# Optimization experiments

Hardware: AMD Instinct MI355X
Metric: run time of the kernel (lower is better)

The kernel has to match this reference:

```python
import jax, jax.numpy as jnp
import numpy as np

STAGE_NUM = 5
BETA = 1.0
EPS = 1e-6


def _em_refine(cls, proto):
    # cls: [b, d]; proto: [k, d]. Matches torch einsum('bd,bkd->bk') with
    # batch-replicated prototypes == cls @ proto.T (no (b,k,d) materialization).
    p = proto
    for _ in range(STAGE_NUM):
        r = jax.nn.softmax(cls @ p.T, axis=1)          # [b, k]
        p = r.T @ cls                                   # [k, d]
        p = p / (jnp.linalg.norm(p, axis=1, keepdims=True) + EPS)
    return p


def setup_inputs() -> dict:
    key = jax.random.key(0)
    k1, k2 = jax.random.split(key)
    b, d, k = 8192, 1024, 512
    cls = jax.random.normal(k1, (b, d), dtype=jnp.float32)
    proto = jax.random.normal(k2, (k, d), dtype=jnp.float32)
    # __init__ normalizes prototypes to unit norm (with 1e-6 in denominator)
    proto = proto / (1e-6 + jnp.linalg.norm(proto, axis=1, keepdims=True))
    return {"cls": cls, "prototypes": proto}


def reference(cls, prototypes):
    # EM loop runs under torch.no_grad() -> stop_gradient here.
    new_proto = jax.lax.stop_gradient(_em_refine(cls, prototypes))  # [k, d]
    dot = cls @ new_proto.T                                          # [b, k]
    r = jax.nn.softmax(dot, axis=1)
    z_recon = r @ new_proto                                          # [b, d]
    z_out = BETA * z_recon + cls
    return (r, z_out)
```

## Files before the change

### kernel.cpp

```cpp
#include <hip/hip_runtime.h>

typedef short v8s __attribute__((ext_vector_type(8)));
typedef _Float16 v8h __attribute__((ext_vector_type(8)));
typedef float v4f __attribute__((ext_vector_type(4)));

typedef __attribute__((address_space(1))) const void* as1_void_cp;
typedef __attribute__((address_space(3))) void* as3_void_p;

__device__ __forceinline__ unsigned short f2bf(float x) {
  union { float f; unsigned int u; } v; v.f = x;
  unsigned int r = v.u + 0x7fffu + ((v.u >> 16) & 1u);
  return (unsigned short)(r >> 16);
}
__device__ __forceinline__ float bf2f(unsigned short h) {
  union { unsigned int u; float f; } v; v.u = ((unsigned int)h) << 16;
  return v.f;
}
__device__ __forceinline__ unsigned short f2h(float x) {
  _Float16 h = (_Float16)x;
  return __builtin_bit_cast(unsigned short, h);
}

template <bool ADD, bool F16>
__global__ __launch_bounds__(256) void gemm_bt(
    const unsigned short* __restrict__ A, const unsigned short* __restrict__ B,
    float* __restrict__ C, const float* __restrict__ Cadd,
    int N, int lda, int ldb, int klen, size_t csplit) {
  __shared__ __align__(16) unsigned short As[128 * 64];
  __shared__ __align__(16) unsigned short Bs[128 * 64];
  const int tid = threadIdx.x;
  const int bn = blockIdx.x * 128, bm = blockIdx.y * 128;
  const int k0 = blockIdx.z * klen;
  float* Cp = C + (size_t)blockIdx.z * csplit;

  const unsigned short* ag0 = A + (size_t)(bm + (tid >> 2)) * lda + ((tid & 3) << 3) + k0;
  const unsigned short* ag1 = ag0 + (size_t)64 * lda;
  const unsigned short* bg0 = B + (size_t)(bn + (tid >> 2)) * ldb + ((tid & 3) << 3) + k0;
  const unsigned short* bg1 = bg0 + (size_t)64 * ldb;
  unsigned short* al0 = As + tid * 8;
  unsigned short* al1 = As + 2048 + tid * 8;
  unsigned short* al2 = As + 4096 + tid * 8;
  unsigned short* al3 = As + 6144 + tid * 8;
  unsigned short* bl0 = Bs + tid * 8;
  unsigned short* bl1 = Bs + 2048 + tid * 8;
  unsigned short* bl2 = Bs + 4096 + tid * 8;
  unsigned short* bl3 = Bs + 6144 + tid * 8;

  const int lane = tid & 63;
  const int q = lane >> 4, m15 = lane & 15;
  const int w = tid >> 6;
  const int wr = (w >> 1) * 64, wc = (w & 1) * 64;

  v4f acc[4][4];
#pragma unroll
  for (int i = 0; i < 4; ++i)
#pragma unroll
    for (int j = 0; j < 4; ++j) acc[i][j] = 0.f;

  for (int kk = 0; kk < klen; kk += 64) {
    __builtin_amdgcn_global_load_lds((as1_void_cp)(ag0 + kk), (as3_void_p)al0, 16, 0, 0);
    __builtin_amdgcn_global_load_lds((as1_void_cp)(ag1 + kk), (as3_void_p)al1, 16, 0, 0);
    __builtin_amdgcn_global_load_lds((as1_void_cp)(ag0 + kk + 32), (as3_void_p)al2, 16, 0, 0);
    __builtin_amdgcn_global_load_lds((as1_void_cp)(ag1 + kk + 32), (as3_void_p)al3, 16, 0, 0);
    __builtin_amdgcn_global_load_lds((as1_void_cp)(bg0 + kk), (as3_void_p)bl0, 16, 0, 0);
    __builtin_amdgcn_global_load_lds((as1_void_cp)(bg1 + kk), (as3_void_p)bl1, 16, 0, 0);
    __builtin_amdgcn_global_load_lds((as1_void_cp)(bg0 + kk + 32), (as3_void_p)bl2, 16, 0, 0);
    __builtin_amdgcn_global_load_lds((as1_void_cp)(bg1 + kk + 32), (as3_void_p)bl3, 16, 0, 0);
    __syncthreads();
#pragma unroll
    for (int h = 0; h < 2; ++h) {
      v8s af[4], bf[4];
#pragma unroll
      for (int i = 0; i < 4; ++i)
        af[i] = *(const v8s*)(As + h * 4096 + (wr + i * 16 + m15) * 32 + q * 8);
#pragma unroll
      for (int j = 0; j < 4; ++j)
        bf[j] = *(const v8s*)(Bs + h * 4096 + (wc + j * 16 + m15) * 32 + q * 8);
#pragma unroll
      for (int i = 0; i < 4; ++i)
#pragma unroll
        for (int j = 0; j < 4; ++j) {
          if constexpr (F16)
            acc[i][j] = __builtin_amdgcn_mfma_f32_16x16x32_f16(
                __builtin_bit_cast(v8h, af[i]), __builtin_bit_cast(v8h, bf[j]), acc[i][j], 0, 0, 0);
          else
            acc[i][j] = __builtin_amdgcn_mfma_f32_16x16x32_bf16(af[i], bf[j], acc[i][j], 0, 0, 0);
        }
    }
    __syncthreads();
  }

#pragma unroll
  for (int i = 0; i < 4; ++i) {
#pragma unroll
    for (int j = 0; j < 4; ++j) {
      const int col = bn + wc + j * 16 + m15;
#pragma unroll
      for (int rr = 0; rr < 4; ++rr) {
        const int row = bm + wr + i * 16 + q * 4 + rr;
        const size_t idx = (size_t)row * N + col;
        float v = acc[i][j][rr];
        if (ADD) v += Cadd[idx];
        Cp[idx] = v;
      }
    }
  }
}

__global__ __launch_bounds__(256) void gemm_bt3(
    const unsigned short* __restrict__ Ah, const unsigned short* __restrict__ Al,
    const unsigned short* __restrict__ Bh, const unsigned short* __restrict__ Bl,
    float* __restrict__ C, int N, int lda, int ldb, int klen, size_t csplit) {
  __shared__ __align__(16) unsigned short Ash[128 * 32];
  __shared__ __align__(16) unsigned short Asl[128 * 32];
  __shared__ __align__(16) unsigned short Bsh[128 * 32];
  __shared__ __align__(16) unsigned short Bsl[128 * 32];
  const int tid = threadIdx.x;
  const int bn = blockIdx.x * 128, bm = blockIdx.y * 128;
  const int k0 = blockIdx.z * klen;
  float* Cp = C + (size_t)blockIdx.z * csplit;

  const size_t aoff = (size_t)(bm + (tid >> 2)) * lda + ((tid & 3) << 3) + k0;
  const size_t boff = (size_t)(bn + (tid >> 2)) * ldb + ((tid & 3) << 3) + k0;
  const unsigned short* agh0 = Ah + aoff;
  const unsigned short* agh1 = agh0 + (size_t)64 * lda;
  const unsigned short* agl0 = Al + aoff;
  const unsigned short* agl1 = agl0 + (size_t)64 * lda;
  const unsigned short* bgh0 = Bh + boff;
  const unsigned short* bgh1 = bgh0 + (size_t)64 * ldb;
  const unsigned short* bgl0 = Bl + boff;
  const unsigned short* bgl1 = bgl0 + (size_t)64 * ldb;

  const int lane = tid & 63;
  const int q = lane >> 4, m15 = lane & 15;
  const int w = tid >> 6;
  const int wr = (w >> 1) * 64, wc = (w & 1) * 64;

  v4f acc[4][4];
#pragma unroll
  for (int i = 0; i < 4; ++i)
#pragma unroll
    for (int j = 0; j < 4; ++j) acc[i][j] = 0.f;

  for (int kk = 0; kk < klen; kk += 32) {
    __builtin_amdgcn_global_load_lds((as1_void_cp)(agh0 + kk), (as3_void_p)(Ash + tid * 8), 16, 0, 0);
    __builtin_amdgcn_global_load_lds((as1_void_cp)(agh1 + kk), (as3_void_p)(Ash + 2048 + tid * 8), 16, 0, 0);
    __builtin_amdgcn_global_load_lds((as1_void_cp)(agl0 + kk), (as3_void_p)(Asl + tid * 8), 16, 0, 0);
    __builtin_amdgcn_global_load_lds((as1_void_cp)(agl1 + kk), (as3_void_p)(Asl + 2048 + tid * 8), 16, 0, 0);
    __builtin_amdgcn_global_load_lds((as1_void_cp)(bgh0 + kk), (as3_void_p)(Bsh + tid * 8), 16, 0, 0);
    __builtin_amdgcn_global_load_lds((as1_void_cp)(bgh1 + kk), (as3_void_p)(Bsh + 2048 + tid * 8), 16, 0, 0);
    __builtin_amdgcn_global_load_lds((as1_void_cp)(bgl0 + kk), (as3_void_p)(Bsl + tid * 8), 16, 0, 0);
    __builtin_amdgcn_global_load_lds((as1_void_cp)(bgl1 + kk), (as3_void_p)(Bsl + 2048 + tid * 8), 16, 0, 0);
    __syncthreads();
    v8s afh[4], afl[4], bfh[4], bfl[4];
#pragma unroll
    for (int i = 0; i < 4; ++i) {
      const int ro = (wr + i * 16 + m15) * 32 + q * 8;
      afh[i] = *(const v8s*)(Ash + ro);
      afl[i] = *(const v8s*)(Asl + ro);
    }
#pragma unroll
    for (int j = 0; j < 4; ++j) {
      const int ro = (wc + j * 16 + m15) * 32 + q * 8;
      bfh[j] = *(const v8s*)(Bsh + ro);
      bfl[j] = *(const v8s*)(Bsl + ro);
    }
#pragma unroll
    for (int i = 0; i < 4; ++i)
#pragma unroll
      for (int j = 0; j < 4; ++j) {
        acc[i][j] = __builtin_amdgcn_mfma_f32_16x16x32_bf16(afh[i], bfh[j], acc[i][j], 0, 0, 0);
        acc[i][j] = __builtin_amdgcn_mfma_f32_16x16x32_bf16(afh[i], bfl[j], acc[i][j], 0, 0, 0);
        acc[i][j] = __builtin_amdgcn_mfma_f32_16x16x32_bf16(afl[i], bfh[j], acc[i][j], 0, 0, 0);
      }
    __syncthreads();
  }

#pragma unroll
  for (int i = 0; i < 4; ++i) {
#pragma unroll
    for (int j = 0; j < 4; ++j) {
      const int col = bn + wc + j * 16 + m15;
#pragma unroll
      for (int rr = 0; rr < 4; ++rr) {
        const int row = bm + wr + i * 16 + q * 4 + rr;
        Cp[(size_t)row * N + col] = acc[i][j][rr];
      }
    }
  }
}

__global__ __launch_bounds__(256) void cast_split_transpose_cls(
    const float* __restrict__ cls,
    unsigned short* __restrict__ ch, unsigned short* __restrict__ cl,
    unsigned short* __restrict__ cTh, unsigned short* __restrict__ cTl) {
  __shared__ unsigned short th[64][72];
  __shared__ unsigned short tl[64][72];
  const int d0 = blockIdx.x * 64, b0 = blockIdx.y * 64;
  const int t = threadIdx.x;
#pragma unroll
  for (int i = 0; i < 4; ++i) {
    int flat = t + i * 256;
    int bl_ = flat >> 4;
    int dl = (flat & 15) << 2;
    float4 v = *(const float4*)(cls + (size_t)(b0 + bl_) * 1024 + d0 + dl);
    ushort4 h, l;
    h.x = f2bf(v.x); l.x = f2bf(v.x - bf2f(h.x));
    h.y = f2bf(v.y); l.y = f2bf(v.y - bf2f(h.y));
    h.z = f2bf(v.z); l.z = f2bf(v.z - bf2f(h.z));
    h.w = f2bf(v.w); l.w = f2bf(v.w - bf2f(h.w));
    *(ushort4*)(ch + (size_t)(b0 + bl_) * 1024 + d0 + dl) = h;
    *(ushort4*)(cl + (size_t)(b0 + bl_) * 1024 + d0 + dl) = l;
    th[bl_][dl] = h.x; th[bl_][dl + 1] = h.y; th[bl_][dl + 2] = h.z; th[bl_][dl + 3] = h.w;
    tl[bl_][dl] = l.x; tl[bl_][dl + 1] = l.y; tl[bl_][dl + 2] = l.z; tl[bl_][dl + 3] = l.w;
  }
  __syncthreads();
#pragma unroll
  for (int i = 0; i < 4; ++i) {
    int flat = t + i * 256;
    int dl = flat >> 4;
    int bl_ = (flat & 15) << 2;
    ushort4 h = make_ushort4(th[bl_][dl], th[bl_ + 1][dl], th[bl_ + 2][dl], th[bl_ + 3][dl]);
    ushort4 l = make_ushort4(tl[bl_][dl], tl[bl_ + 1][dl], tl[bl_ + 2][dl], tl[bl_ + 3][dl]);
    *(ushort4*)(cTh + (size_t)(d0 + dl) * 8192 + b0 + bl_) = h;
    *(ushort4*)(cTl + (size_t)(d0 + dl) * 8192 + b0 + bl_) = l;
  }
}

__global__ __launch_bounds__(256) void split_f32(const float* __restrict__ in,
                                                 unsigned short* __restrict__ hi,
                                                 unsigned short* __restrict__ lo) {
  const size_t i = (size_t)(blockIdx.x * blockDim.x + threadIdx.x) * 4;
  float4 v = *(const float4*)(in + i);
  ushort4 h, l;
  h.x = f2bf(v.x); l.x = f2bf(v.x - bf2f(h.x));
  h.y = f2bf(v.y); l.y = f2bf(v.y - bf2f(h.y));
  h.z = f2bf(v.z); l.z = f2bf(v.z - bf2f(h.z));
  h.w = f2bf(v.w); l.w = f2bf(v.w - bf2f(h.w));
  *(ushort4*)(hi + i) = h;
  *(ushort4*)(lo + i) = l;
}

__global__ __launch_bounds__(256) void fuse_to_f16_dual(
    const unsigned short* __restrict__ h0, const unsigned short* __restrict__ l0,
    unsigned short* __restrict__ o0,
    const unsigned short* __restrict__ h1, const unsigned short* __restrict__ l1,
    unsigned short* __restrict__ o1) {
  const int half = blockIdx.x >> 12;
  const unsigned short* hi = half ? h1 : h0;
  const unsigned short* lo = half ? l1 : l0;
  unsigned short* out = half ? o1 : o0;
  const size_t i = ((size_t)(blockIdx.x & 4095) * 256 + threadIdx.x) * 8;
  ushort4 ha = *(const ushort4*)(hi + i);
  ushort4 hb = *(const ushort4*)(hi + i + 4);
  ushort4 la = *(const ushort4*)(lo + i);
  ushort4 lb = *(const ushort4*)(lo + i + 4);
  ushort4 oa, ob;
  oa.x = f2h(bf2f(ha.x) + bf2f(la.x)); oa.y = f2h(bf2f(ha.y) + bf2f(la.y));
  oa.z = f2h(bf2f(ha.z) + bf2f(la.z)); oa.w = f2h(bf2f(ha.w) + bf2f(la.w));
  ob.x = f2h(bf2f(hb.x) + bf2f(lb.x)); ob.y = f2h(bf2f(hb.y) + bf2f(lb.y));
  ob.z = f2h(bf2f(hb.z) + bf2f(lb.z)); ob.w = f2h(bf2f(hb.w) + bf2f(lb.w));
  *(ushort4*)(out + i) = oa;
  *(ushort4*)(out + i + 4) = ob;
}

template <bool HILO>
__global__ __launch_bounds__(512) void rowsoftmax_T(
    const float* __restrict__ SP0, const float* __restrict__ SP1,
    unsigned short* __restrict__ rTh, unsigned short* __restrict__ rTl) {
  __shared__ __align__(16) unsigned short th[32 * 520];
  __shared__ __align__(16) unsigned short tl[HILO ? 32 * 520 : 8];
  const int t = threadIdx.x;
  const int lane = t & 63, w = t >> 6;
  const int b0 = blockIdx.x * 32;
#pragma unroll
  for (int k = 0; k < 4; ++k) {
    const int bl = w * 4 + k;
    const int row = b0 + bl;
    const size_t off = (size_t)row * 512 + lane * 8;
    float4 v0 = *(const float4*)(SP0 + off);
    float4 v1 = *(const float4*)(SP0 + off + 4);
    float4 u0 = *(const float4*)(SP1 + off);
    float4 u1 = *(const float4*)(SP1 + off + 4);
    float e[8];
    e[0] = v0.x + u0.x; e[1] = v0.y + u0.y; e[2] = v0.z + u0.z; e[3] = v0.w + u0.w;
    e[4] = v1.x + u1.x; e[5] = v1.y + u1.y; e[6] = v1.z + u1.z; e[7] = v1.w + u1.w;
    float m = fmaxf(fmaxf(fmaxf(e[0], e[1]), fmaxf(e[2], e[3])),
                    fmaxf(fmaxf(e[4], e[5]), fmaxf(e[6], e[7])));
    for (int o = 32; o; o >>= 1) m = fmaxf(m, __shfl_xor(m, o));
    float s = 0.f;
#pragma unroll
    for (int i = 0; i < 8; ++i) { e[i] = __expf(e[i] - m); s += e[i]; }
    for (int o = 32; o; o >>= 1) s += __shfl_xor(s, o);
    const float inv = 1.f / s;
    unsigned short ph[8], pl[8];
#pragma unroll
    for (int i = 0; i < 8; ++i) {
      const float r = e[i] * inv;
      if constexpr (HILO) {
        ph[i] = f2bf(r);
        pl[i] = f2bf(r - bf2f(ph[i]));
      } else {
        ph[i] = f2h(r);
      }
    }
    *(v8s*)&th[bl * 520 + lane * 8] = *(v8s*)ph;
    if constexpr (HILO) *(v8s*)&tl[bl * 520 + lane * 8] = *(v8s*)pl;
  }
  __syncthreads();
  const int c = t;
  unsigned short uh[32];
#pragma unroll
  for (int b = 0; b < 32; ++b) uh[b] = th[b * 520 + c];
#pragma unroll
  for (int q = 0; q < 4; ++q)
    *(v8s*)(rTh + (size_t)c * 8192 + b0 + q * 8) = *(v8s*)&uh[q * 8];
  if constexpr (HILO) {
    unsigned short ul[32];
#pragma unroll
    for (int b = 0; b < 32; ++b) ul[b] = tl[b * 520 + c];
#pragma unroll
    for (int q = 0; q < 4; ++q)
      *(v8s*)(rTl + (size_t)c * 8192 + b0 + q * 8) = *(v8s*)&ul[q * 8];
  }
}

__global__ __launch_bounds__(256) void softmax_rows(const float* __restrict__ SP0,
                                                    const float* __restrict__ SP1,
                                                    float* __restrict__ r_out,
                                                    unsigned short* __restrict__ r_g) {
  const int w = threadIdx.x >> 6, lane = threadIdx.x & 63;
  const int row = blockIdx.x * 4 + w;
  const size_t off = (size_t)row * 512 + lane * 8;
  float4 v0 = *(const float4*)(SP0 + off);
  float4 v1 = *(const float4*)(SP0 + off + 4);
  float4 u0 = *(const float4*)(SP1 + off);
  float4 u1 = *(const float4*)(SP1 + off + 4);
  v0.x += u0.x; v0.y += u0.y; v0.z += u0.z; v0.w += u0.w;
  v1.x += u1.x; v1.y += u1.y; v1.z += u1.z; v1.w += u1.w;
  float m = fmaxf(fmaxf(fmaxf(v0.x, v0.y), fmaxf(v0.z, v0.w)),
                  fmaxf(fmaxf(v1.x, v1.y), fmaxf(v1.z, v1.w)));
  for (int off2 = 32; off2; off2 >>= 1) m = fmaxf(m, __shfl_xor(m, off2));
  float e0 = __expf(v0.x - m), e1 = __expf(v0.y - m), e2 = __expf(v0.z - m), e3 = __expf(v0.w - m);
  float e4 = __expf(v1.x - m), e5 = __expf(v1.y - m), e6 = __expf(v1.z - m), e7 = __expf(v1.w - m);
  float s = e0 + e1 + e2 + e3 + e4 + e5 + e6 + e7;
  for (int off2 = 32; off2; off2 >>= 1) s += __shfl_xor(s, off2);
  const float inv = 1.f / s;
  e0 *= inv; e1 *= inv; e2 *= inv; e3 *= inv; e4 *= inv; e5 *= inv; e6 *= inv; e7 *= inv;
  float* rp = r_out + off;
  *(float4*)rp = make_float4(e0, e1, e2, e3);
  *(float4*)(rp + 4) = make_float4(e4, e5, e6, e7);
  unsigned short* bp = r_g + off;
  *(ushort4*)bp = make_ushort4(f2h(e0), f2h(e1), f2h(e2), f2h(e3));
  *(ushort4*)(bp + 4) = make_ushort4(f2h(e4), f2h(e5), f2h(e6), f2h(e7));
}

__global__ __launch_bounds__(256) void reduce_normalize(const float* __restrict__ Pp,
                                                        unsigned short* __restrict__ pg,
                                                        unsigned short* __restrict__ pTg) {
  __shared__ float red[4];
  const int c = blockIdx.x, t = threadIdx.x;
  float ax = 0.f, ay = 0.f, az = 0.f, aw = 0.f;
#pragma unroll
  for (int s = 0; s < 16; ++s) {
    const float4 v = *(const float4*)(Pp + ((size_t)s * 512 + c) * 1024 + t * 4);
    ax += v.x; ay += v.y; az += v.z; aw += v.w;
  }
  float ss = ax * ax + ay * ay + az * az + aw * aw;
  for (int off = 32; off; off >>= 1) ss += __shfl_xor(ss, off);
  const int w = t >> 6, lane = t & 63;
  if (!lane) red[w] = ss;
  __syncthreads();
  const float tot = red[0] + red[1] + red[2] + red[3];
  const float scale = 1.f / (sqrtf(tot) + 1e-6f);
  ax *= scale; ay *= scale; az *= scale; aw *= scale;
  *(ushort4*)(pg + (size_t)c * 1024 + t * 4) =
      make_ushort4(f2h(ax), f2h(ay), f2h(az), f2h(aw));
  pTg[(size_t)(t * 4 + 0) * 512 + c] = f2h(ax);
  pTg[(size_t)(t * 4 + 1) * 512 + c] = f2h(ay);
  pTg[(size_t)(t * 4 + 2) * 512 + c] = f2h(az);
  pTg[(size_t)(t * 4 + 3) * 512 + c] = f2h(aw);
}

__global__ __launch_bounds__(256) void reduce_normalize_hl(const float* __restrict__ Pp,
                                                           unsigned short* __restrict__ ph,
                                                           unsigned short* __restrict__ pl) {
  __shared__ float red[4];
  const int c = blockIdx.x, t = threadIdx.x;
  float ax = 0.f, ay = 0.f, az = 0.f, aw = 0.f;
#pragma unroll
  for (int s = 0; s < 16; ++s) {
    const float4 v = *(const float4*)(Pp + ((size_t)s * 512 + c) * 1024 + t * 4);
    ax += v.x; ay += v.y; az += v.z; aw += v.w;
  }
  float ss = ax * ax + ay * ay + az * az + aw * aw;
  for (int off = 32; off; off >>= 1) ss += __shfl_xor(ss, off);
  const int w = t >> 6, lane = t & 63;
  if (!lane) red[w] = ss;
  __syncthreads();
  const float tot = red[0] + red[1] + red[2] + red[3];
  const float scale = 1.f / (sqrtf(tot) + 1e-6f);
  ax *= scale; ay *= scale; az *= scale; aw *= scale;
  ushort4 h, l;
  h.x = f2bf(ax); l.x = f2bf(ax - bf2f(h.x));
  h.y = f2bf(ay); l.y = f2bf(ay - bf2f(h.y));
  h.z = f2bf(az); l.z = f2bf(az - bf2f(h.z));
  h.w = f2bf(aw); l.w = f2bf(aw - bf2f(h.w));
  *(ushort4*)(ph + (size_t)c * 1024 + t * 4) = h;
  *(ushort4*)(pl + (size_t)c * 1024 + t * 4) = l;
}

extern "C" void kernel_launch(void* const* d_in, const int* in_sizes, int n_in,
                              void* d_out, int out_size, void* d_ws, size_t ws_size,
                              hipStream_t stream) {
  const float* cls = (const float*)d_in[0];
  const float* proto = (const float*)d_in[1];
  float* out_r = (float*)d_out;
  float* out_z = out_r + (size_t)8192 * 512;

  char* w = (char*)d_ws;
  unsigned short* cls_h = (unsigned short*)w; w += (size_t)8192 * 1024 * 2;
  unsigned short* cls_l = (unsigned short*)w; w += (size_t)8192 * 1024 * 2;
  unsigned short* clsT_h = (unsigned short*)w; w += (size_t)1024 * 8192 * 2;
  unsigned short* clsT_l = (unsigned short*)w; w += (size_t)1024 * 8192 * 2;
  unsigned short* p_h = (unsigned short*)w; w += (size_t)512 * 1024 * 2;
  unsigned short* p_l = (unsigned short*)w; w += (size_t)512 * 1024 * 2;
  unsigned short* p_g = (unsigned short*)w; w += (size_t)512 * 1024 * 2;
  unsigned short* pT_g = (unsigned short*)w; w += (size_t)1024 * 512 * 2;
  unsigned short* rT_h = (unsigned short*)w; w += (size_t)512 * 8192 * 2;
  unsigned short* rT_l = (unsigned short*)w; w += (size_t)512 * 8192 * 2;
  float* SP = (float*)w;
  float* SP1 = SP + (size_t)8192 * 512;
  unsigned short* cls_g = cls_l;
  unsigned short* clsT_g = clsT_l;

  cast_split_transpose_cls<<<dim3(16, 128), 256, 0, stream>>>(cls, cls_h, cls_l, clsT_h, clsT_l);
  split_f32<<<512, 256, 0, stream>>>(proto, p_h, p_l);

  gemm_bt3<<<dim3(4, 64, 2), 256, 0, stream>>>(cls_h, cls_l, p_h, p_l, SP,
                                               512, 1024, 1024, 512,
                                               (size_t)8192 * 512);
  rowsoftmax_T<true><<<256, 512, 0, stream>>>(SP, SP1, rT_h, rT_l);
  gemm_bt3<<<dim3(8, 4, 16), 256, 0, stream>>>(rT_h, rT_l, clsT_h, clsT_l, SP,
                                               1024, 8192, 8192, 512,
                                               (size_t)512 * 1024);
  fuse_to_f16_dual<<<8192, 256, 0, stream>>>(cls_h, cls_l, cls_g, clsT_h, clsT_l, clsT_g);
  reduce_normalize<<<512, 256, 0, stream>>>(SP, p_g, pT_g);

  for (int it = 0; it < 4; ++it) {
    gemm_bt<false, true><<<dim3(4, 64, 2), 256, 0, stream>>>(cls_g, p_g, SP, nullptr,
                                                             512, 1024, 1024, 512,
                                                             (size_t)8192 * 512);
    rowsoftmax_T<false><<<256, 512, 0, stream>>>(SP, SP1, rT_h, nullptr);
    gemm_bt<false, true><<<dim3(8, 4, 16), 256, 0, stream>>>(rT_h, clsT_g, SP, nullptr,
                                                             1024, 8192, 8192, 512,
                                                             (size_t)512 * 1024);
    reduce_normalize<<<512, 256, 0, stream>>>(SP, p_g, pT_g);
  }

  gemm_bt<false, true><<<dim3(4, 64, 2), 256, 0, stream>>>(cls_g, p_g, SP, nullptr,
                                                           512, 1024, 1024, 512,
                                                           (size_t)8192 * 512);
  softmax_rows<<<2048, 256, 0, stream>>>(SP, SP1, out_r, rT_h);
  gemm_bt<true, true><<<dim3(8, 64, 1), 256, 0, stream>>>(rT_h, pT_g, out_z, cls,
                                                          1024, 512, 512, 512, 0);
}
```

Measured before the change: 489.0 us.

## Fuse score GEMM with row softmax and emit fp16 cls during cast

Replaces the split-K score GEMM plus separate softmax/transpose kernels with one kernel. Each 512-thread block computes a 32x512 score tile directly from global memory using f16 MFMA, does the row softmax in registers and shared memory, and writes either the transposed fp16 responsibilities or the final fp32 r. The fp16 copies of cls and its transpose are now produced inside the initial cast kernel, which removes the separate fuse pass. The aim is to cut the fp32 score round trip through memory and several launches. The trade-off is that the fused GEMM has only 256 blocks, does no LDS staging and makes redundant global loads of B, so its efficiency is uncertain.

```diff
diff --git a/kernel.cpp b/kernel.cpp
--- a/kernel.cpp
+++ b/kernel.cpp
@@ -193,7 +193,8 @@
 __global__ __launch_bounds__(256) void cast_split_transpose_cls(
     const float* __restrict__ cls,
     unsigned short* __restrict__ ch, unsigned short* __restrict__ cl,
-    unsigned short* __restrict__ cTh, unsigned short* __restrict__ cTl) {
+    unsigned short* __restrict__ cTh, unsigned short* __restrict__ cTl,
+    unsigned short* __restrict__ cg, unsigned short* __restrict__ cTg) {
   __shared__ unsigned short th[64][72];
   __shared__ unsigned short tl[64][72];
   const int d0 = blockIdx.x * 64, b0 = blockIdx.y * 64;
@@ -204,13 +205,14 @@
     int bl_ = flat >> 4;
     int dl = (flat & 15) << 2;
     float4 v = *(const float4*)(cls + (size_t)(b0 + bl_) * 1024 + d0 + dl);
-    ushort4 h, l;
-    h.x = f2bf(v.x); l.x = f2bf(v.x - bf2f(h.x));
-    h.y = f2bf(v.y); l.y = f2bf(v.y - bf2f(h.y));
-    h.z = f2bf(v.z); l.z = f2bf(v.z - bf2f(h.z));
-    h.w = f2bf(v.w); l.w = f2bf(v.w - bf2f(h.w));
+    ushort4 h, l, g;
+    h.x = f2bf(v.x); l.x = f2bf(v.x - bf2f(h.x)); g.x = f2h(v.x);
+    h.y = f2bf(v.y); l.y = f2bf(v.y - bf2f(h.y)); g.y = f2h(v.y);
+    h.z = f2bf(v.z); l.z = f2bf(v.z - bf2f(h.z)); g.z = f2h(v.z);
+    h.w = f2bf(v.w); l.w = f2bf(v.w - bf2f(h.w)); g.w = f2h(v.w);
     *(ushort4*)(ch + (size_t)(b0 + bl_) * 1024 + d0 + dl) = h;
     *(ushort4*)(cl + (size_t)(b0 + bl_) * 1024 + d0 + dl) = l;
+    *(ushort4*)(cg + (size_t)(b0 + bl_) * 1024 + d0 + dl) = g;
     th[bl_][dl] = h.x; th[bl_][dl + 1] = h.y; th[bl_][dl + 2] = h.z; th[bl_][dl + 3] = h.w;
     tl[bl_][dl] = l.x; tl[bl_][dl + 1] = l.y; tl[bl_][dl + 2] = l.z; tl[bl_][dl + 3] = l.w;
   }
@@ -222,8 +224,14 @@
     int bl_ = (flat & 15) << 2;
     ushort4 h = make_ushort4(th[bl_][dl], th[bl_ + 1][dl], th[bl_ + 2][dl], th[bl_ + 3][dl]);
     ushort4 l = make_ushort4(tl[bl_][dl], tl[bl_ + 1][dl], tl[bl_ + 2][dl], tl[bl_ + 3][dl]);
+    ushort4 g;
+    g.x = f2h(bf2f(h.x) + bf2f(l.x));
+    g.y = f2h(bf2f(h.y) + bf2f(l.y));
+    g.z = f2h(bf2f(h.z) + bf2f(l.z));
+    g.w = f2h(bf2f(h.w) + bf2f(l.w));
     *(ushort4*)(cTh + (size_t)(d0 + dl) * 8192 + b0 + bl_) = h;
     *(ushort4*)(cTl + (size_t)(d0 + dl) * 8192 + b0 + bl_) = l;
+    *(ushort4*)(cTg + (size_t)(d0 + dl) * 8192 + b0 + bl_) = g;
   }
 }
 
@@ -239,29 +247,6 @@
   h.w = f2bf(v.w); l.w = f2bf(v.w - bf2f(h.w));
   *(ushort4*)(hi + i) = h;
   *(ushort4*)(lo + i) = l;
-}
-
-__global__ __launch_bounds__(256) void fuse_to_f16_dual(
-    const unsigned short* __restrict__ h0, const unsigned short* __restrict__ l0,
-    unsigned short* __restrict__ o0,
-    const unsigned short* __restrict__ h1, const unsigned short* __restrict__ l1,
-    unsigned short* __restrict__ o1) {
-  const int half = blockIdx.x >> 12;
-  const unsigned short* hi = half ? h1 : h0;
-  const unsigned short* lo = half ? l1 : l0;
-  unsigned short* out = half ? o1 : o0;
-  const size_t i = ((size_t)(blockIdx.x & 4095) * 256 + threadIdx.x) * 8;
-  ushort4 ha = *(const ushort4*)(hi + i);
-  ushort4 hb = *(const ushort4*)(hi + i + 4);
-  ushort4 la = *(const ushort4*)(lo + i);
-  ushort4 lb = *(const ushort4*)(lo + i + 4);
-  ushort4 oa, ob;
-  oa.x = f2h(bf2f(ha.x) + bf2f(la.x)); oa.y = f2h(bf2f(ha.y) + bf2f(la.y));
-  oa.z = f2h(bf2f(ha.z) + bf2f(la.z)); oa.w = f2h(bf2f(ha.w) + bf2f(la.w));
-  ob.x = f2h(bf2f(hb.x) + bf2f(lb.x)); ob.y = f2h(bf2f(hb.y) + bf2f(lb.y));
-  ob.z = f2h(bf2f(hb.z) + bf2f(lb.z)); ob.w = f2h(bf2f(hb.w) + bf2f(lb.w));
-  *(ushort4*)(out + i) = oa;
-  *(ushort4*)(out + i + 4) = ob;
 }
 
 template <bool HILO>
@@ -325,34 +310,155 @@
   }
 }
 
-__global__ __launch_bounds__(256) void softmax_rows(const float* __restrict__ SP0,
-                                                    const float* __restrict__ SP1,
-                                                    float* __restrict__ r_out,
-                                                    unsigned short* __restrict__ r_g) {
-  const int w = threadIdx.x >> 6, lane = threadIdx.x & 63;
-  const int row = blockIdx.x * 4 + w;
-  const size_t off = (size_t)row * 512 + lane * 8;
-  float4 v0 = *(const float4*)(SP0 + off);
-  float4 v1 = *(const float4*)(SP0 + off + 4);
-  float4 u0 = *(const float4*)(SP1 + off);
-  float4 u1 = *(const float4*)(SP1 + off + 4);
-  v0.x += u0.x; v0.y += u0.y; v0.z += u0.z; v0.w += u0.w;
-  v1.x += u1.x; v1.y += u1.y; v1.z += u1.z; v1.w += u1.w;
-  float m = fmaxf(fmaxf(fmaxf(v0.x, v0.y), fmaxf(v0.z, v0.w)),
-                  fmaxf(fmaxf(v1.x, v1.y), fmaxf(v1.z, v1.w)));
-  for (int off2 = 32; off2; off2 >>= 1) m = fmaxf(m, __shfl_xor(m, off2));
-  float e0 = __expf(v0.x - m), e1 = __expf(v0.y - m), e2 = __expf(v0.z - m), e3 = __expf(v0.w - m);
-  float e4 = __expf(v1.x - m), e5 = __expf(v1.y - m), e6 = __expf(v1.z - m), e7 = __expf(v1.w - m);
-  float s = e0 + e1 + e2 + e3 + e4 + e5 + e6 + e7;
-  for (int off2 = 32; off2; off2 >>= 1) s += __shfl_xor(s, off2);
-  const float inv = 1.f / s;
-  e0 *= inv; e1 *= inv; e2 *= inv; e3 *= inv; e4 *= inv; e5 *= inv; e6 *= inv; e7 *= inv;
-  float* rp = r_out + off;
-  *(float4*)rp = make_float4(e0, e1, e2, e3);
-  *(float4*)(rp + 4) = make_float4(e4, e5, e6, e7);
-  unsigned short* bp = r_g + off;
-  *(ushort4*)bp = make_ushort4(f2h(e0), f2h(e1), f2h(e2), f2h(e3));
-  *(ushort4*)(bp + 4) = make_ushort4(f2h(e4), f2h(e5), f2h(e6), f2h(e7));
+template <bool FINAL>
+__global__ __launch_bounds__(512, 2) void s_softmax_fused(
+    const unsigned short* __restrict__ A,
+    const unsigned short* __restrict__ B,
+    unsigned short* __restrict__ rT,
+    float* __restrict__ r_out,
+    unsigned short* __restrict__ r_row) {
+  __shared__ float redm[8][32];
+  __shared__ float reds[8][32];
+  __shared__ __align__(16) unsigned short th[32 * 520];
+  const int tid = threadIdx.x;
+  const int lane = tid & 63;
+  const int w = tid >> 6;
+  const int q = lane >> 4, m15 = lane & 15;
+  const int b0 = blockIdx.x * 32;
+
+  const unsigned short* a0 = A + (size_t)(b0 + m15) * 1024 + q * 8;
+  const unsigned short* a1 = a0 + (size_t)16 * 1024;
+  const unsigned short* bp0 = B + (size_t)(w * 64 + m15) * 1024 + q * 8;
+  const unsigned short* bp1 = bp0 + (size_t)16 * 1024;
+  const unsigned short* bp2 = bp0 + (size_t)32 * 1024;
+  const unsigned short* bp3 = bp0 + (size_t)48 * 1024;
+
+  v4f acc[2][4];
+#pragma unroll
+  for (int i = 0; i < 2; ++i)
+#pragma unroll
+    for (int j = 0; j < 4; ++j) acc[i][j] = 0.f;
+
+  for (int kk = 0; kk < 1024; kk += 64) {
+    v8s a00 = *(const v8s*)(a0 + kk);
+    v8s a01 = *(const v8s*)(a0 + kk + 32);
+    v8s a10 = *(const v8s*)(a1 + kk);
+    v8s a11 = *(const v8s*)(a1 + kk + 32);
+    v8s b00 = *(const v8s*)(bp0 + kk);
+    v8s b01 = *(const v8s*)(bp0 + kk + 32);
+    v8s b10 = *(const v8s*)(bp1 + kk);
+    v8s b11 = *(const v8s*)(bp1 + kk + 32);
+    v8s b20 = *(const v8s*)(bp2 + kk);
+    v8s b21 = *(const v8s*)(bp2 + kk + 32);
+    v8s b30 = *(const v8s*)(bp3 + kk);
+    v8s b31 = *(const v8s*)(bp3 + kk + 32);
+#define MF(ii, jj, av, bv) \
+    acc[ii][jj] = __builtin_amdgcn_mfma_f32_16x16x32_f16( \
+        __builtin_bit_cast(v8h, av), __builtin_bit_cast(v8h, bv), acc[ii][jj], 0, 0, 0)
+    MF(0, 0, a00, b00); MF(0, 1, a00, b10); MF(0, 2, a00, b20); MF(0, 3, a00, b30);
+    MF(1, 0, a10, b00); MF(1, 1, a10, b10); MF(1, 2, a10, b20); MF(1, 3, a10, b30);
+    MF(0, 0, a01, b01); MF(0, 1, a01, b11); MF(0, 2, a01, b21); MF(0, 3, a01, b31);
+    MF(1, 0, a11, b01); MF(1, 1, a11, b11); MF(1, 2, a11, b21); MF(1, 3, a11, b31);
+#undef MF
+  }
+
+  float mx[2][4];
+#pragma unroll
+  for (int i = 0; i < 2; ++i)
+#pragma unroll
+    for (int rr = 0; rr < 4; ++rr) {
+      float m = fmaxf(fmaxf(acc[i][0][rr], acc[i][1][rr]),
+                      fmaxf(acc[i][2][rr], acc[i][3][rr]));
+      m = fmaxf(m, __shfl_xor(m, 1));
+      m = fmaxf(m, __shfl_xor(m, 2));
+      m = fmaxf(m, __shfl_xor(m, 4));
+      m = fmaxf(m, __shfl_xor(m, 8));
+      mx[i][rr] = m;
+    }
+  if (m15 == 0) {
+#pragma unroll
+    for (int i = 0; i < 2; ++i)
+#pragma unroll
+      for (int rr = 0; rr < 4; ++rr) redm[w][i * 16 + q * 4 + rr] = mx[i][rr];
+  }
+  __syncthreads();
+#pragma unroll
+  for (int i = 0; i < 2; ++i)
+#pragma unroll
+    for (int rr = 0; rr < 4; ++rr) {
+      const int row = i * 16 + q * 4 + rr;
+      float m = redm[0][row];
+#pragma unroll
+      for (int ww = 1; ww < 8; ++ww) m = fmaxf(m, redm[ww][row]);
+      mx[i][rr] = m;
+    }
+
+  float sm[2][4];
+#pragma unroll
+  for (int i = 0; i < 2; ++i)
+#pragma unroll
+    for (int rr = 0; rr < 4; ++rr) {
+      float s = 0.f;
+#pragma unroll
+      for (int j = 0; j < 4; ++j) {
+        const float e = __expf(acc[i][j][rr] - mx[i][rr]);
+        acc[i][j][rr] = e;
+        s += e;
+      }
+      s += __shfl_xor(s, 1);
+      s += __shfl_xor(s, 2);
+      s += __shfl_xor(s, 4);
+      s += __shfl_xor(s, 8);
+      sm[i][rr] = s;
+    }
+  if (m15 == 0) {
+#pragma unroll
+    for (int i = 0; i < 2; ++i)
+#pragma unroll
+      for (int rr = 0; rr < 4; ++rr) reds[w][i * 16 + q * 4 + rr] = sm[i][rr];
+  }
+  __syncthreads();
+#pragma unroll
+  for (int i = 0; i < 2; ++i)
+#pragma unroll
+    for (int rr = 0; rr < 4; ++rr) {
+      const int row = i * 16 + q * 4 + rr;
+      float s = reds[0][row];
+#pragma unroll
+      for (int ww = 1; ww < 8; ++ww) s += reds[ww][row];
+      sm[i][rr] = 1.f / s;
+    }
+
+#pragma unroll
+  for (int i = 0; i < 2; ++i)
+#pragma unroll
+    for (int j = 0; j < 4; ++j)
+#pragma unroll
+      for (int rr = 0; rr < 4; ++rr) {
+        const float v = acc[i][j][rr] * sm[i][rr];
+        const int row = i * 16 + q * 4 + rr;
+        const int col = w * 64 + j * 16 + m15;
+        th[row * 520 + col] = f2h(v);
+        if constexpr (FINAL) r_out[(size_t)(b0 + row) * 512 + col] = v;
+      }
+  __syncthreads();
+
+  if constexpr (!FINAL) {
+    const int c = tid;
+    unsigned short uh[32];
+#pragma unroll
+    for (int b = 0; b < 32; ++b) uh[b] = th[b * 520 + c];
+#pragma unroll
+    for (int t4 = 0; t4 < 4; ++t4)
+      *(v8s*)(rT + (size_t)c * 8192 + b0 + t4 * 8) = *(v8s*)&uh[t4 * 8];
+  } else {
+    const int row = tid >> 4;
+    const int c0 = (tid & 15) * 32;
+#pragma unroll
+    for (int t4 = 0; t4 < 4; ++t4)
+      *(v8s*)(r_row + (size_t)(b0 + row) * 512 + c0 + t4 * 8) =
+          *(const v8s*)&th[row * 520 + c0 + t4 * 8];
+  }
 }
 
 __global__ __launch_bounds__(256) void reduce_normalize(const float* __restrict__ Pp,
@@ -382,34 +488,6 @@
   pTg[(size_t)(t * 4 + 3) * 512 + c] = f2h(aw);
 }
 
-__global__ __launch_bounds__(256) void reduce_normalize_hl(const float* __restrict__ Pp,
-                                                           unsigned short* __restrict__ ph,
-                                                           unsigned short* __restrict__ pl) {
-  __shared__ float red[4];
-  const int c = blockIdx.x, t = threadIdx.x;
-  float ax = 0.f, ay = 0.f, az = 0.f, aw = 0.f;
-#pragma unroll
-  for (int s = 0; s < 16; ++s) {
-    const float4 v = *(const float4*)(Pp + ((size_t)s * 512 + c) * 1024 + t * 4);
-    ax += v.x; ay += v.y; az += v.z; aw += v.w;
-  }
-  float ss = ax * ax + ay * ay + az * az + aw * aw;
-  for (int off = 32; off; off >>= 1) ss += __shfl_xor(ss, off);
-  const int w = t >> 6, lane = t & 63;
-  if (!lane) red[w] = ss;
-  __syncthreads();
-  const float tot = red[0] + red[1] + red[2] + red[3];
-  const float scale = 1.f / (sqrtf(tot) + 1e-6f);
-  ax *= scale; ay *= scale; az *= scale; aw *= scale;
-  ushort4 h, l;
-  h.x = f2bf(ax); l.x = f2bf(ax - bf2f(h.x));
-  h.y = f2bf(ay); l.y = f2bf(ay - bf2f(h.y));
-  h.z = f2bf(az); l.z = f2bf(az - bf2f(h.z));
-  h.w = f2bf(aw); l.w = f2bf(aw - bf2f(h.w));
-  *(ushort4*)(ph + (size_t)c * 1024 + t * 4) = h;
-  *(ushort4*)(pl + (size_t)c * 1024 + t * 4) = l;
-}
-
 extern "C" void kernel_launch(void* const* d_in, const int* in_sizes, int n_in,
                               void* d_out, int out_size, void* d_ws, size_t ws_size,
                               hipStream_t stream) {
@@ -423,6 +501,8 @@
   unsigned short* cls_l = (unsigned short*)w; w += (size_t)8192 * 1024 * 2;
   unsigned short* clsT_h = (unsigned short*)w; w += (size_t)1024 * 8192 * 2;
   unsigned short* clsT_l = (unsigned short*)w; w += (size_t)1024 * 8192 * 2;
+  unsigned short* cls_g = (unsigned short*)w; w += (size_t)8192 * 1024 * 2;
+  unsigned short* clsT_g = (unsigned short*)w; w += (size_t)1024 * 8192 * 2;
   unsigned short* p_h = (unsigned short*)w; w += (size_t)512 * 1024 * 2;
   unsigned short* p_l = (unsigned short*)w; w += (size_t)512 * 1024 * 2;
   unsigned short* p_g = (unsigned short*)w; w += (size_t)512 * 1024 * 2;
@@ -431,10 +511,9 @@
   unsigned short* rT_l = (unsigned short*)w; w += (size_t)512 * 8192 * 2;
   float* SP = (float*)w;
   float* SP1 = SP + (size_t)8192 * 512;
-  unsigned short* cls_g = cls_l;
-  unsigned short* clsT_g = clsT_l;
-
-  cast_split_transpose_cls<<<dim3(16, 128), 256, 0, stream>>>(cls, cls_h, cls_l, clsT_h, clsT_l);
+
+  cast_split_transpose_cls<<<dim3(16, 128), 256, 0, stream>>>(
+      cls, cls_h, cls_l, clsT_h, clsT_l, cls_g, clsT_g);
   split_f32<<<512, 256, 0, stream>>>(proto, p_h, p_l);
 
   gemm_bt3<<<dim3(4, 64, 2), 256, 0, stream>>>(cls_h, cls_l, p_h, p_l, SP,
@@ -444,24 +523,17 @@
   gemm_bt3<<<dim3(8, 4, 16), 256, 0, stream>>>(rT_h, rT_l, clsT_h, clsT_l, SP,
                                                1024, 8192, 8192, 512,
                                                (size_t)512 * 1024);
-  fuse_to_f16_dual<<<8192, 256, 0, stream>>>(cls_h, cls_l, cls_g, clsT_h, clsT_l, clsT_g);
   reduce_normalize<<<512, 256, 0, stream>>>(SP, p_g, pT_g);
 
   for (int it = 0; it < 4; ++it) {
-    gemm_bt<false, true><<<dim3(4, 64, 2), 256, 0, stream>>>(cls_g, p_g, SP, nullptr,
-                                                             512, 1024, 1024, 512,
-                                                             (size_t)8192 * 512);
-    rowsoftmax_T<false><<<256, 512, 0, stream>>>(SP, SP1, rT_h, nullptr);
+    s_softmax_fused<false><<<256, 512, 0, stream>>>(cls_g, p_g, rT_h, nullptr, nullptr);
     gemm_bt<false, true><<<dim3(8, 4, 16), 256, 0, stream>>>(rT_h, clsT_g, SP, nullptr,
                                                              1024, 8192, 8192, 512,
                                                              (size_t)512 * 1024);
     reduce_normalize<<<512, 256, 0, stream>>>(SP, p_g, pT_g);
   }
 
-  gemm_bt<false, true><<<dim3(4, 64, 2), 256, 0, stream>>>(cls_g, p_g, SP, nullptr,
-                                                           512, 1024, 1024, 512,
-                                                           (size_t)8192 * 512);
-  softmax_rows<<<2048, 256, 0, stream>>>(SP, SP1, out_r, rT_h);
+  s_softmax_fused<true><<<256, 512, 0, stream>>>(cls_g, p_g, nullptr, out_r, rT_h);
   gemm_bt<true, true><<<dim3(8, 64, 1), 256, 0, stream>>>(rT_h, pT_g, out_z, cls,
                                                           1024, 512, 512, 512, 0);
 }
```

New measurement: 586.9 us. 1.2x slower.
